# Kernel optimization log

Measured on AMD Instinct MI355X. Metric: run time of the kernel, lower is better.

## Reference

```python
import jax, jax.numpy as jnp
import numpy as np

HEADS = 8
DIM_HEAD = 64
QUERY_DIM = 1024
CONTEXT_DIM = 768
INNER = HEADS * DIM_HEAD  # 512


def setup_inputs() -> dict:
    key = jax.random.key(0)
    ks = jax.random.split(key, 8)
    b, n, j = 4, 2048, 2048
    x = jax.random.normal(ks[0], (b, n, QUERY_DIM), dtype=jnp.float32)
    context = jax.random.normal(ks[1], (b, j, CONTEXT_DIM), dtype=jnp.float32)
    mask = jax.random.randint(ks[2], (b, j), 0, 2).astype(jnp.bool_)
    # weights stored as (in, out) so forward is x @ W (torch Linear stores transpose)
    W_q = jax.random.normal(ks[3], (QUERY_DIM, INNER), dtype=jnp.float32) / np.sqrt(QUERY_DIM)
    W_k = jax.random.normal(ks[4], (CONTEXT_DIM, INNER), dtype=jnp.float32) / np.sqrt(CONTEXT_DIM)
    W_v = jax.random.normal(ks[5], (CONTEXT_DIM, INNER), dtype=jnp.float32) / np.sqrt(CONTEXT_DIM)
    W_o = jax.random.normal(ks[6], (INNER, QUERY_DIM), dtype=jnp.float32) / np.sqrt(INNER)
    b_o = jax.random.normal(ks[7], (QUERY_DIM,), dtype=jnp.float32) * 0.01
    return {"x": x, "context": context, "mask": mask,
            "W_q": W_q, "W_k": W_k, "W_v": W_v, "W_o": W_o, "b_o": b_o}


def reference(x, context, mask, W_q, W_k, W_v, W_o, b_o):
    b, n, _ = x.shape
    j = context.shape[1]
    scale = DIM_HEAD ** -0.5
    # projections -> [b, n, h, d]
    q = (x @ W_q).reshape(b, n, HEADS, DIM_HEAD)
    k = (context @ W_k).reshape(b, j, HEADS, DIM_HEAD)
    v = (context @ W_v).reshape(b, j, HEADS, DIM_HEAD)
    # similarity [b, h, n, j]
    sim = jnp.einsum('bihd,bjhd->bhij', q, k) * scale
    max_neg = -jnp.finfo(sim.dtype).max
    sim = jnp.where(mask[:, None, None, :], sim, max_neg)
    attn = jax.nn.softmax(sim, axis=-1)
    out = jnp.einsum('bhij,bjhd->bihd', attn, v).reshape(b, n, INNER)
    return out @ W_o + b_o  # dropout is identity (p=0 / eval)
```

## Files before the change

### kernel.cpp

```cpp
#include <hip/hip_runtime.h>
#include <hip/hip_bf16.h>

typedef __attribute__((ext_vector_type(4)))  float  f32x4;
typedef __attribute__((ext_vector_type(16))) float  f32x16;
typedef __attribute__((ext_vector_type(8)))  short  bf16x8;
typedef __attribute__((ext_vector_type(4)))  int    int32x4;
typedef __attribute__((ext_vector_type(2)))  unsigned int uint32x2;

#define DEVINL static __device__ __forceinline__
#define GAS __attribute__((address_space(1)))
#define LAS __attribute__((address_space(3)))

DEVINL ushort f2bf(float f) {
  unsigned u = __builtin_bit_cast(unsigned, f);
  unsigned r = u + 0x7fffu + ((u >> 16) & 1u);
  return (ushort)(r >> 16);
}

DEVINL unsigned cvtpk(float lo, float hi) {
  unsigned r;
  asm("v_cvt_pk_bf16_f32 %0, %1, %2" : "=v"(r) : "v"(lo), "v"(hi));
  return r;
}

DEVINL void plswap(unsigned &a, unsigned &b) {
  asm("v_permlane32_swap_b32 %0, %1" : "+v"(a), "+v"(b));
}

DEVINL float fexp2(float x) { return __builtin_amdgcn_exp2f(x); }

DEVINL float bf2f(short s) {
  return __builtin_bit_cast(float, ((unsigned)(ushort)s) << 16);
}

DEVINL f32x4 mfma16(bf16x8 a, bf16x8 b, f32x4 c) {
  return __builtin_amdgcn_mfma_f32_16x16x32_bf16(a, b, c, 0, 0, 0);
}
DEVINL f32x16 mfma32(bf16x8 a, bf16x8 b, f32x16 c) {
  return __builtin_amdgcn_mfma_f32_32x32x16_bf16(a, b, c, 0, 0, 0);
}

__global__ __launch_bounds__(256)
void prep_k(const float* __restrict__ x, const float* __restrict__ ctx,
            ushort* __restrict__ xb, ushort* __restrict__ cb,
            const int* __restrict__ msk, float* __restrict__ mbias,
            const float* __restrict__ Wq, const float* __restrict__ Wk,
            const float* __restrict__ Wv, const float* __restrict__ Wo,
            ushort* __restrict__ WqT, ushort* __restrict__ WkT,
            ushort* __restrict__ WvT, ushort* __restrict__ WoT)
{
  __shared__ ushort Ts[64][72];
  int id = blockIdx.x;
  if (id < 448) {
    const float* src; ushort* dst; int Kd, Nd, lid;
    if (id < 128)      { src = Wq; dst = WqT; Kd = 1024; Nd = 512;  lid = id; }
    else if (id < 224) { src = Wk; dst = WkT; Kd = 768;  Nd = 512;  lid = id - 128; }
    else if (id < 320) { src = Wv; dst = WvT; Kd = 768;  Nd = 512;  lid = id - 224; }
    else               { src = Wo; dst = WoT; Kd = 512;  Nd = 1024; lid = id - 320; }
    const int sh = (Nd == 512) ? 3 : 4;
    const int kb = lid >> sh, nb = lid & ((1 << sh) - 1);
    const int k0 = kb * 64, n0 = nb * 64;
    const int t = threadIdx.x;
    const int r = t >> 2, c0 = (t & 3) * 16;

    const float* sp = src + (size_t)(k0 + r) * Nd + n0 + c0;
    f32x4 v0 = *(const f32x4*)(sp);
    f32x4 v1 = *(const f32x4*)(sp + 4);
    f32x4 v2 = *(const f32x4*)(sp + 8);
    f32x4 v3 = *(const f32x4*)(sp + 12);
    #pragma unroll
    for (int e = 0; e < 4; e++) {
      Ts[c0 + e][r]      = f2bf(v0[e]);
      Ts[c0 + 4 + e][r]  = f2bf(v1[e]);
      Ts[c0 + 8 + e][r]  = f2bf(v2[e]);
      Ts[c0 + 12 + e][r] = f2bf(v3[e]);
    }
    __syncthreads();
    const int n = t >> 2, kc = (t & 3) * 16;
    bf16x8 o0 = *(const bf16x8*)&Ts[n][kc];
    bf16x8 o1 = *(const bf16x8*)&Ts[n][kc + 8];
    ushort* dp = dst + (size_t)(n0 + n) * Kd + k0 + kc;
    *(bf16x8*)dp       = o0;
    *(bf16x8*)(dp + 8) = o1;
    return;
  }

  const int NX = 8388608, NC = 6291456;
  int tid = (id - 448) * 256 + threadIdx.x;
  if (tid < 8192) mbias[tid] = msk[tid] ? 0.f : -1e30f;
  for (int i = tid; i < (NX + NC) / 8; i += 2048 * 256) {
    int e = i * 8;
    const float* s; ushort* d;
    if (e < NX) { s = x + e; d = xb + e; }
    else        { s = ctx + (e - NX); d = cb + (e - NX); }
    f32x4 v0 = *(const f32x4*)s;
    f32x4 v1 = *(const f32x4*)(s + 4);
    union { unsigned u[4]; int32x4 v; } pk;
    pk.u[0] = cvtpk(v0[0], v0[1]);
    pk.u[1] = cvtpk(v0[2], v0[3]);
    pk.u[2] = cvtpk(v1[0], v1[1]);
    pk.u[3] = cvtpk(v1[2], v1[3]);
    *(int32x4*)d = pk.v;
  }
}

template<int PHASE>
__global__ __launch_bounds__(256)
void mm_k(const ushort* __restrict__ xb, const ushort* __restrict__ cb,
          const ushort* __restrict__ WqT, const ushort* __restrict__ WkT,
          const ushort* __restrict__ WvT,
          ushort* __restrict__ Qb, ushort* __restrict__ Kb, ushort* __restrict__ VT,
          const ushort* __restrict__ AO, const ushort* __restrict__ WoT,
          float* __restrict__ out, const float* __restrict__ bias)
{
  __shared__ ushort As[2][128 * 32];
  __shared__ ushort Bs[2][128 * 32];

  const ushort* A; const ushort* BT; ushort* Cw = nullptr;
  int Kd, mode, m0, n0;
  if (PHASE == 0) {
    int id = blockIdx.x;
    id = (id & 7) * 96 + (id >> 3);
    const int which = id >> 8, local = id & 255;
    m0 = (local >> 2) * 128; n0 = (local & 3) * 128;
    if (which == 0)      { A = xb; BT = WqT; Cw = Qb; Kd = 1024; mode = 1; }
    else if (which == 1) { A = cb; BT = WkT; Cw = Kb; Kd = 768;  mode = 1; }
    else                 { A = cb; BT = WvT; Cw = VT; Kd = 768;  mode = 2; }
  } else {
    int id = blockIdx.x;
    id = (id & 7) * 64 + (id >> 3);
    m0 = (id >> 3) * 128; n0 = (id & 7) * 128;
    A = AO; BT = WoT; Kd = 512; mode = 0;
  }

  const int t = threadIdx.x, lane = t & 63, w = t >> 6;
  const int wr = w >> 1, wc = w & 1;
  const int g = lane >> 4, ql = lane & 15;

  const int srowo = 16 * w + (lane >> 2);
  const int sgg = (lane & 3) ^ ((lane >> 3) & 3);

  f32x4 acc[4][4];
  #pragma unroll
  for (int i = 0; i < 4; i++)
    #pragma unroll
    for (int j = 0; j < 4; j++) acc[i][j] = (f32x4){0.f, 0.f, 0.f, 0.f};

  auto stage = [&](int buf, int k0) {
    #pragma unroll
    for (int i = 0; i < 2; i++) {
      const int row = i * 64 + srowo;
      const ushort* asrc = A + (size_t)(m0 + row) * Kd + k0 + sgg * 8;
      __builtin_amdgcn_global_load_lds((const GAS void*)asrc,
          (LAS void*)&As[buf][(i * 64 + 16 * w) * 32], 16, 0, 0);
      const ushort* bsrc = BT + (size_t)(n0 + row) * Kd + k0 + sgg * 8;
      __builtin_amdgcn_global_load_lds((const GAS void*)bsrc,
          (LAS void*)&Bs[buf][(i * 64 + 16 * w) * 32], 16, 0, 0);
    }
  };

  const int NK = Kd >> 5;
  stage(0, 0);
  __syncthreads();

  const int sel = (ql >> 1) & 3;
  const int koff = (g ^ sel) * 8;

  for (int tt = 0; tt < NK; tt++) {
    const int cur = tt & 1;
    if (tt + 1 < NK) stage(cur ^ 1, (tt + 1) * 32);

    bf16x8 af[4], bfr[4];
    #pragma unroll
    for (int i = 0; i < 4; i++) {
      af[i]  = *(const bf16x8*)&As[cur][(wr * 64 + i * 16 + ql) * 32 + koff];
      bfr[i] = *(const bf16x8*)&Bs[cur][(wc * 64 + i * 16 + ql) * 32 + koff];
    }
    #pragma unroll
    for (int i = 0; i < 4; i++)
      #pragma unroll
      for (int j = 0; j < 4; j++)
        acc[i][j] = mfma16(af[i], bfr[j], acc[i][j]);
    __syncthreads();
  }

  #pragma unroll
  for (int i = 0; i < 4; i++) {
    #pragma unroll
    for (int j = 0; j < 4; j++) {
      int col = n0 + wc * 64 + j * 16 + ql;
      #pragma unroll
      for (int r = 0; r < 4; r++) {
        int mrow = m0 + wr * 64 + i * 16 + g * 4 + r;
        float v = acc[i][j][r];
        if (PHASE == 1) {
          out[(size_t)mrow * 1024 + col] = v + bias[col];
        } else {
          int b = mrow >> 11, nn = mrow & 2047;
          int hh = col >> 6, dd = col & 63;
          size_t base = (size_t)(b * 8 + hh) * 131072;
          if (mode == 1) Cw[base + (size_t)nn * 64 + dd]   = f2bf(v);
          else           Cw[base + (size_t)dd * 2048 + nn] = f2bf(v);
        }
      }
    }
  }
}

__global__ __launch_bounds__(512)
void attn_k(const ushort* __restrict__ Qb, const ushort* __restrict__ Kb,
            const ushort* __restrict__ VT, const float* __restrict__ mb,
            ushort* __restrict__ Opart, float2* __restrict__ Ml)
{
  constexpr int CHUNK = 512, NT = CHUNK / 64;
  __shared__ ushort Ks[2][64 * 64];
  __shared__ ushort Vs[2][64 * 64];

  const int bh = blockIdx.x, b = bh >> 3;
  const int sp = blockIdx.z;
  const int jb = sp * CHUNK;
  const int t = threadIdx.x, lane = t & 63, w = t >> 6;
  const int l31 = lane & 31, hi = lane >> 5;
  const int q0 = blockIdx.y * 256 + w * 32;

  const ushort* Qh = Qb + (size_t)bh * 131072;
  const ushort* Kh = Kb + (size_t)bh * 131072;
  const ushort* Vh = VT + (size_t)bh * 131072;
  const float* mp = mb + b * 2048 + 4 * hi;

  const int srow = lane >> 3;
  const int soff = ((lane & 7) * 16) ^ ((srow & 7) << 4);

  auto stage = [&](int buf, int j0) {
    const char* kg = (const char*)Kh + ((size_t)(j0 + 8 * w + srow)) * 128 + soff;
    __builtin_amdgcn_global_load_lds((const GAS void*)kg,
        (LAS void*)&Ks[buf][8 * w * 64], 16, 0, 0);
    const char* vg = (const char*)Vh + ((size_t)(8 * w + srow)) * 4096 + (size_t)j0 * 2 + soff;
    __builtin_amdgcn_global_load_lds((const GAS void*)vg,
        (LAS void*)&Vs[buf][8 * w * 64], 16, 0, 0);
  };

  bf16x8 qf[4];
  #pragma unroll
  for (int kk = 0; kk < 4; kk++)
    qf[kk] = *(const bf16x8*)(Qh + (size_t)(q0 + l31) * 64 + kk * 16 + 8 * hi);

  union { unsigned u[4]; bf16x8 v; } ones;
  ones.u[0] = 0x3F803F80u; ones.u[1] = 0x3F803F80u;
  ones.u[2] = 0x3F803F80u; ones.u[3] = 0x3F803F80u;

  f32x16 o0 = {}, o1 = {};
  float m = -1e30f, lsum = 0.f;
  const float sc = 0.18033688011112042f;

  stage(0, jb);
  __syncthreads();

  for (int tt = 0; tt < NT; ++tt) {
    const int cur = tt & 1;
    if (tt + 1 < NT) stage(cur ^ 1, jb + (tt + 1) * 64);

    #pragma unroll
    for (int js = 0; js < 2; ++js) {
      const int jloc = js * 32;
      const int j0 = jb + tt * 64 + jloc;

      f32x4 mb0 = *(const f32x4*)(mp + j0);
      f32x4 mb1 = *(const f32x4*)(mp + j0 + 8);
      f32x4 mb2 = *(const f32x4*)(mp + j0 + 16);
      f32x4 mb3 = *(const f32x4*)(mp + j0 + 24);

      const int krow = jloc + l31;
      const unsigned rsw = (unsigned)((l31 & 7) << 4);
      const char* kbase = (const char*)&Ks[cur][0] + krow * 128;
      bf16x8 kf0 = *(const bf16x8*)(kbase + ((0  + hi * 16) ^ rsw));
      bf16x8 kf1 = *(const bf16x8*)(kbase + ((32 + hi * 16) ^ rsw));
      bf16x8 kf2 = *(const bf16x8*)(kbase + ((64 + hi * 16) ^ rsw));
      bf16x8 kf3 = *(const bf16x8*)(kbase + ((96 + hi * 16) ^ rsw));

      __builtin_amdgcn_s_setprio(1);
      f32x16 z = {};
      f32x16 s = mfma32(kf0, qf[0], z);
      s = mfma32(kf1, qf[1], s);
      s = mfma32(kf2, qf[2], s);
      s = mfma32(kf3, qf[3], s);
      __builtin_amdgcn_s_setprio(0);

      const char* vb0 = (const char*)&Vs[cur][0] + l31 * 128;
      const char* vb1 = vb0 + 32 * 128;
      const unsigned vc0 = (unsigned)((jloc * 2 + hi * 16) ^ rsw);
      const unsigned vc1 = (unsigned)((jloc * 2 + 32 + hi * 16) ^ rsw);
      bf16x8 vf00 = *(const bf16x8*)(vb0 + vc0);
      bf16x8 vf01 = *(const bf16x8*)(vb0 + vc1);
      bf16x8 vf10 = *(const bf16x8*)(vb1 + vc0);
      bf16x8 vf11 = *(const bf16x8*)(vb1 + vc1);

      float pv[16];
      #pragma unroll
      for (int e = 0; e < 4; e++) {
        pv[e]      = fmaf(s[e],      sc, mb0[e]);
        pv[4 + e]  = fmaf(s[4 + e],  sc, mb1[e]);
        pv[8 + e]  = fmaf(s[8 + e],  sc, mb2[e]);
        pv[12 + e] = fmaf(s[12 + e], sc, mb3[e]);
      }

      float t0 = fmaxf(fmaxf(pv[0],  pv[1]),  pv[2]);
      float t1 = fmaxf(fmaxf(pv[3],  pv[4]),  pv[5]);
      float t2 = fmaxf(fmaxf(pv[6],  pv[7]),  pv[8]);
      float t3 = fmaxf(fmaxf(pv[9],  pv[10]), pv[11]);
      float t4 = fmaxf(fmaxf(pv[12], pv[13]), pv[14]);
      float pm = fmaxf(fmaxf(fmaxf(t0, t1), t2), fmaxf(fmaxf(t3, t4), pv[15]));
      pm = fmaxf(pm, __shfl_xor(pm, 32));

      if (!__all(pm <= m + 8.f)) {
        float mn = fmaxf(m, pm);
        float al = fexp2(m - mn);
        lsum *= al;
        #pragma unroll
        for (int r = 0; r < 16; r++) { o0[r] *= al; o1[r] *= al; }
        m = mn;
      }

      #pragma unroll
      for (int r = 0; r < 16; r++) pv[r] = fexp2(pv[r] - m);

      unsigned pk01 = cvtpk(pv[0],  pv[1]),  pk23 = cvtpk(pv[2],  pv[3]);
      unsigned pk45 = cvtpk(pv[4],  pv[5]),  pk67 = cvtpk(pv[6],  pv[7]);
      unsigned pk89 = cvtpk(pv[8],  pv[9]),  pkAB = cvtpk(pv[10], pv[11]);
      unsigned pkCD = cvtpk(pv[12], pv[13]), pkEF = cvtpk(pv[14], pv[15]);
      plswap(pk01, pk45);
      plswap(pk23, pk67);
      plswap(pk89, pkCD);
      plswap(pkAB, pkEF);
      union { unsigned u[4]; bf16x8 v; } pf0, pf1;
      pf0.u[0] = pk01; pf0.u[1] = pk23; pf0.u[2] = pk45; pf0.u[3] = pk67;
      pf1.u[0] = pk89; pf1.u[1] = pkAB; pf1.u[2] = pkCD; pf1.u[3] = pkEF;

      __builtin_amdgcn_s_setprio(1);
      f32x16 zs = {};
      zs = mfma32(ones.v, pf0.v, zs);
      zs = mfma32(ones.v, pf1.v, zs);
      o0 = mfma32(vf00, pf0.v, o0);
      o0 = mfma32(vf01, pf1.v, o0);
      o1 = mfma32(vf10, pf0.v, o1);
      o1 = mfma32(vf11, pf1.v, o1);
      __builtin_amdgcn_s_setprio(0);
      lsum += zs[0];
    }
    __syncthreads();
  }

  float inv = lsum > 0.f ? 1.0f / lsum : 0.f;
  const int q = q0 + l31;
  ushort* op = Opart + (size_t)sp * 4194304 + ((size_t)(bh * 2048 + q)) * 64;
  #pragma unroll
  for (int grp = 0; grp < 4; grp++) {
    int d0 = grp * 8 + 4 * hi;
    uint32x2 w0, w1;
    w0[0] = cvtpk(o0[4 * grp] * inv, o0[4 * grp + 1] * inv);
    w0[1] = cvtpk(o0[4 * grp + 2] * inv, o0[4 * grp + 3] * inv);
    w1[0] = cvtpk(o1[4 * grp] * inv, o1[4 * grp + 1] * inv);
    w1[1] = cvtpk(o1[4 * grp + 2] * inv, o1[4 * grp + 3] * inv);
    *(uint32x2*)(op + d0)      = w0;
    *(uint32x2*)(op + 32 + d0) = w1;
  }
  if (hi == 0) {
    float2 v; v.x = m; v.y = lsum;
    Ml[sp * 65536 + bh * 2048 + q] = v;
  }
}

__global__ __launch_bounds__(256)
void reduce_k(const ushort* __restrict__ Opart, const float2* __restrict__ Ml,
              ushort* __restrict__ AO)
{
  const int idx = blockIdx.x * 256 + threadIdx.x;
  const int d8 = idx & 7, q = (idx >> 3) & 2047, bh = idx >> 14;
  const int b = bh >> 3, h = bh & 7;

  float2 ml[4];
  float M = -1e30f;
  #pragma unroll
  for (int s = 0; s < 4; s++) {
    ml[s] = Ml[s * 65536 + bh * 2048 + q];
    M = fmaxf(M, ml[s].x);
  }
  float wgt[4], L = 0.f;
  #pragma unroll
  for (int s = 0; s < 4; s++) {
    wgt[s] = ml[s].y * fexp2(ml[s].x - M);
    L += wgt[s];
  }
  float invL = 1.f / L;

  float acc[8] = {0.f,0.f,0.f,0.f,0.f,0.f,0.f,0.f};
  #pragma unroll
  for (int s = 0; s < 4; s++) {
    bf16x8 v = *(const bf16x8*)(Opart + (size_t)s * 4194304 +
                                ((size_t)(bh * 2048 + q)) * 64 + d8 * 8);
    float ws = wgt[s] * invL;
    #pragma unroll
    for (int e = 0; e < 8; e++) acc[e] += ws * bf2f(v[e]);
  }

  union { unsigned u[4]; int32x4 v; } pk;
  pk.u[0] = cvtpk(acc[0], acc[1]);
  pk.u[1] = cvtpk(acc[2], acc[3]);
  pk.u[2] = cvtpk(acc[4], acc[5]);
  pk.u[3] = cvtpk(acc[6], acc[7]);
  *(int32x4*)(AO + ((size_t)(b * 2048 + q)) * 512 + h * 64 + d8 * 8) = pk.v;
}

extern "C" void kernel_launch(void* const* d_in, const int* in_sizes, int n_in,
                              void* d_out, int out_size, void* d_ws, size_t ws_size,
                              hipStream_t stream)
{
  const float* x   = (const float*)d_in[0];
  const float* ctx = (const float*)d_in[1];
  const int*   mk  = (const int*)d_in[2];
  const float* Wq  = (const float*)d_in[3];
  const float* Wk  = (const float*)d_in[4];
  const float* Wv  = (const float*)d_in[5];
  const float* Wo  = (const float*)d_in[6];
  const float* bo  = (const float*)d_in[7];
  float* out = (float*)d_out;

  ushort* Qb  = (ushort*)d_ws;
  ushort* Kb  = Qb + 4194304;
  ushort* VT  = Kb + 4194304;
  ushort* WoT = VT + 4194304;
  float*  mb  = (float*)(WoT + 524288);
  ushort* R2  = WoT + 524288 + 16384;
  ushort* xb  = R2;
  ushort* cb  = xb + 8388608;
  ushort* WqT = cb + 6291456;
  ushort* WkT = WqT + 524288;
  ushort* WvT = WkT + 393216;
  ushort* Opart = R2;
  float2* Ml    = (float2*)(R2 + 16777216);
  ushort* AO    = Qb;

  prep_k<<<2496, 256, 0, stream>>>(x, ctx, xb, cb, mk, mb,
                                   Wq, Wk, Wv, Wo, WqT, WkT, WvT, WoT);
  mm_k<0><<<768, 256, 0, stream>>>(xb, cb, WqT, WkT, WvT, Qb, Kb, VT,
                                   nullptr, nullptr, nullptr, nullptr);
  attn_k<<<dim3(32, 8, 4), 512, 0, stream>>>(Qb, Kb, VT, mb, Opart, Ml);
  reduce_k<<<2048, 256, 0, stream>>>(Opart, Ml, AO);
  mm_k<1><<<512, 256, 0, stream>>>(nullptr, nullptr, nullptr, nullptr, nullptr,
                                   nullptr, nullptr, nullptr, AO, WoT, out, bo);
}
```

Baseline: 148.3 us.

## Fuse fp32-to-bf16 activation conversion into projection GEMM A-tile loading

Removes the separate pass that converted x and context to bf16 in prep_k. The phase-0 GEMM now loads fp32 activations directly into registers, converts them with packed cvt instructions, and writes them to a padded LDS tile after the MFMA work, with register prefetch for the next k-step. This drops a full write and re-read of the bf16 activation buffers. In exchange, the GEMM reads twice the bytes for A, which are now read once per N-tile (4 times for Q/K/V) instead of once in the conversion pass. It also uses more registers and replaces async global-to-LDS loads for A with synchronous ones.

```diff
diff --git a/kernel.cpp b/kernel.cpp
--- a/kernel.cpp
+++ b/kernel.cpp
@@ -41,9 +41,7 @@
 }
 
 __global__ __launch_bounds__(256)
-void prep_k(const float* __restrict__ x, const float* __restrict__ ctx,
-            ushort* __restrict__ xb, ushort* __restrict__ cb,
-            const int* __restrict__ msk, float* __restrict__ mbias,
+void prep_k(const int* __restrict__ msk, float* __restrict__ mbias,
             const float* __restrict__ Wq, const float* __restrict__ Wk,
             const float* __restrict__ Wv, const float* __restrict__ Wo,
             ushort* __restrict__ WqT, ushort* __restrict__ WkT,
@@ -51,92 +49,79 @@
 {
   __shared__ ushort Ts[64][72];
   int id = blockIdx.x;
-  if (id < 448) {
-    const float* src; ushort* dst; int Kd, Nd, lid;
-    if (id < 128)      { src = Wq; dst = WqT; Kd = 1024; Nd = 512;  lid = id; }
-    else if (id < 224) { src = Wk; dst = WkT; Kd = 768;  Nd = 512;  lid = id - 128; }
-    else if (id < 320) { src = Wv; dst = WvT; Kd = 768;  Nd = 512;  lid = id - 224; }
-    else               { src = Wo; dst = WoT; Kd = 512;  Nd = 1024; lid = id - 320; }
-    const int sh = (Nd == 512) ? 3 : 4;
-    const int kb = lid >> sh, nb = lid & ((1 << sh) - 1);
-    const int k0 = kb * 64, n0 = nb * 64;
-    const int t = threadIdx.x;
-    const int r = t >> 2, c0 = (t & 3) * 16;
-
-    const float* sp = src + (size_t)(k0 + r) * Nd + n0 + c0;
-    f32x4 v0 = *(const f32x4*)(sp);
-    f32x4 v1 = *(const f32x4*)(sp + 4);
-    f32x4 v2 = *(const f32x4*)(sp + 8);
-    f32x4 v3 = *(const f32x4*)(sp + 12);
-    #pragma unroll
-    for (int e = 0; e < 4; e++) {
-      Ts[c0 + e][r]      = f2bf(v0[e]);
-      Ts[c0 + 4 + e][r]  = f2bf(v1[e]);
-      Ts[c0 + 8 + e][r]  = f2bf(v2[e]);
-      Ts[c0 + 12 + e][r] = f2bf(v3[e]);
-    }
-    __syncthreads();
-    const int n = t >> 2, kc = (t & 3) * 16;
-    bf16x8 o0 = *(const bf16x8*)&Ts[n][kc];
-    bf16x8 o1 = *(const bf16x8*)&Ts[n][kc + 8];
-    ushort* dp = dst + (size_t)(n0 + n) * Kd + k0 + kc;
-    *(bf16x8*)dp       = o0;
-    *(bf16x8*)(dp + 8) = o1;
+  if (id >= 448) {
+    int tid = (id - 448) * 256 + threadIdx.x;
+    if (tid < 8192) mbias[tid] = msk[tid] ? 0.f : -1e30f;
     return;
   }
-
-  const int NX = 8388608, NC = 6291456;
-  int tid = (id - 448) * 256 + threadIdx.x;
-  if (tid < 8192) mbias[tid] = msk[tid] ? 0.f : -1e30f;
-  for (int i = tid; i < (NX + NC) / 8; i += 2048 * 256) {
-    int e = i * 8;
-    const float* s; ushort* d;
-    if (e < NX) { s = x + e; d = xb + e; }
-    else        { s = ctx + (e - NX); d = cb + (e - NX); }
-    f32x4 v0 = *(const f32x4*)s;
-    f32x4 v1 = *(const f32x4*)(s + 4);
-    union { unsigned u[4]; int32x4 v; } pk;
-    pk.u[0] = cvtpk(v0[0], v0[1]);
-    pk.u[1] = cvtpk(v0[2], v0[3]);
-    pk.u[2] = cvtpk(v1[0], v1[1]);
-    pk.u[3] = cvtpk(v1[2], v1[3]);
-    *(int32x4*)d = pk.v;
-  }
+  const float* src; ushort* dst; int Kd, Nd, lid;
+  if (id < 128)      { src = Wq; dst = WqT; Kd = 1024; Nd = 512;  lid = id; }
+  else if (id < 224) { src = Wk; dst = WkT; Kd = 768;  Nd = 512;  lid = id - 128; }
+  else if (id < 320) { src = Wv; dst = WvT; Kd = 768;  Nd = 512;  lid = id - 224; }
+  else               { src = Wo; dst = WoT; Kd = 512;  Nd = 1024; lid = id - 320; }
+  const int sh = (Nd == 512) ? 3 : 4;
+  const int kb = lid >> sh, nb = lid & ((1 << sh) - 1);
+  const int k0 = kb * 64, n0 = nb * 64;
+  const int t = threadIdx.x;
+  const int r = t >> 2, c0 = (t & 3) * 16;
+
+  const float* sp = src + (size_t)(k0 + r) * Nd + n0 + c0;
+  f32x4 v0 = *(const f32x4*)(sp);
+  f32x4 v1 = *(const f32x4*)(sp + 4);
+  f32x4 v2 = *(const f32x4*)(sp + 8);
+  f32x4 v3 = *(const f32x4*)(sp + 12);
+  #pragma unroll
+  for (int e = 0; e < 4; e++) {
+    Ts[c0 + e][r]      = f2bf(v0[e]);
+    Ts[c0 + 4 + e][r]  = f2bf(v1[e]);
+    Ts[c0 + 8 + e][r]  = f2bf(v2[e]);
+    Ts[c0 + 12 + e][r] = f2bf(v3[e]);
+  }
+  __syncthreads();
+  const int n = t >> 2, kc = (t & 3) * 16;
+  bf16x8 o0 = *(const bf16x8*)&Ts[n][kc];
+  bf16x8 o1 = *(const bf16x8*)&Ts[n][kc + 8];
+  ushort* dp = dst + (size_t)(n0 + n) * Kd + k0 + kc;
+  *(bf16x8*)dp       = o0;
+  *(bf16x8*)(dp + 8) = o1;
 }
 
 template<int PHASE>
 __global__ __launch_bounds__(256)
-void mm_k(const ushort* __restrict__ xb, const ushort* __restrict__ cb,
+void mm_k(const float* __restrict__ xf, const float* __restrict__ cf,
           const ushort* __restrict__ WqT, const ushort* __restrict__ WkT,
           const ushort* __restrict__ WvT,
           ushort* __restrict__ Qb, ushort* __restrict__ Kb, ushort* __restrict__ VT,
           const ushort* __restrict__ AO, const ushort* __restrict__ WoT,
           float* __restrict__ out, const float* __restrict__ bias)
 {
-  __shared__ ushort As[2][128 * 32];
+  constexpr int AST = (PHASE == 0) ? 40 : 32;
+  __shared__ ushort As[2][128 * AST];
   __shared__ ushort Bs[2][128 * 32];
 
-  const ushort* A; const ushort* BT; ushort* Cw = nullptr;
+  const float* Af = nullptr; const ushort* Ab = nullptr; const ushort* BT;
+  ushort* Cw = nullptr;
   int Kd, mode, m0, n0;
   if (PHASE == 0) {
     int id = blockIdx.x;
     id = (id & 7) * 96 + (id >> 3);
     const int which = id >> 8, local = id & 255;
     m0 = (local >> 2) * 128; n0 = (local & 3) * 128;
-    if (which == 0)      { A = xb; BT = WqT; Cw = Qb; Kd = 1024; mode = 1; }
-    else if (which == 1) { A = cb; BT = WkT; Cw = Kb; Kd = 768;  mode = 1; }
-    else                 { A = cb; BT = WvT; Cw = VT; Kd = 768;  mode = 2; }
+    if (which == 0)      { Af = xf; BT = WqT; Cw = Qb; Kd = 1024; mode = 1; }
+    else if (which == 1) { Af = cf; BT = WkT; Cw = Kb; Kd = 768;  mode = 1; }
+    else                 { Af = cf; BT = WvT; Cw = VT; Kd = 768;  mode = 2; }
   } else {
     int id = blockIdx.x;
     id = (id & 7) * 64 + (id >> 3);
     m0 = (id >> 3) * 128; n0 = (id & 7) * 128;
-    A = AO; BT = WoT; Kd = 512; mode = 0;
+    Ab = AO; BT = WoT; Kd = 512; mode = 0;
   }
 
   const int t = threadIdx.x, lane = t & 63, w = t >> 6;
   const int wr = w >> 1, wc = w & 1;
   const int g = lane >> 4, ql = lane & 15;
 
+  const int arow = t >> 1, akc = (t & 1) * 16;
   const int srowo = 16 * w + (lane >> 2);
   const int sgg = (lane & 3) ^ ((lane >> 3) & 3);
 
@@ -146,21 +131,49 @@
     #pragma unroll
     for (int j = 0; j < 4; j++) acc[i][j] = (f32x4){0.f, 0.f, 0.f, 0.f};
 
-  auto stage = [&](int buf, int k0) {
+  auto stageB = [&](int buf, int k0) {
     #pragma unroll
     for (int i = 0; i < 2; i++) {
       const int row = i * 64 + srowo;
-      const ushort* asrc = A + (size_t)(m0 + row) * Kd + k0 + sgg * 8;
-      __builtin_amdgcn_global_load_lds((const GAS void*)asrc,
-          (LAS void*)&As[buf][(i * 64 + 16 * w) * 32], 16, 0, 0);
       const ushort* bsrc = BT + (size_t)(n0 + row) * Kd + k0 + sgg * 8;
       __builtin_amdgcn_global_load_lds((const GAS void*)bsrc,
           (LAS void*)&Bs[buf][(i * 64 + 16 * w) * 32], 16, 0, 0);
     }
   };
+  auto stageA_lds = [&](int buf, int k0) {
+    #pragma unroll
+    for (int i = 0; i < 2; i++) {
+      const int row = i * 64 + srowo;
+      const ushort* asrc = Ab + (size_t)(m0 + row) * Kd + k0 + sgg * 8;
+      __builtin_amdgcn_global_load_lds((const GAS void*)asrc,
+          (LAS void*)&As[buf][(i * 64 + 16 * w) * 32], 16, 0, 0);
+    }
+  };
+  auto writeA_f32 = [&](int buf, const f32x4& v0, const f32x4& v1,
+                        const f32x4& v2, const f32x4& v3) {
+    union { unsigned u[4]; int32x4 v; } w1_, w2_;
+    w1_.u[0] = cvtpk(v0[0], v0[1]); w1_.u[1] = cvtpk(v0[2], v0[3]);
+    w1_.u[2] = cvtpk(v1[0], v1[1]); w1_.u[3] = cvtpk(v1[2], v1[3]);
+    w2_.u[0] = cvtpk(v2[0], v2[1]); w2_.u[1] = cvtpk(v2[2], v2[3]);
+    w2_.u[2] = cvtpk(v3[0], v3[1]); w2_.u[3] = cvtpk(v3[2], v3[3]);
+    ushort* dst = &As[buf][arow * 40 + akc];
+    *(int32x4*)dst       = w1_.v;
+    *(int32x4*)(dst + 8) = w2_.v;
+  };
 
   const int NK = Kd >> 5;
-  stage(0, 0);
+  if (PHASE == 0) {
+    const float* ap = Af + (size_t)(m0 + arow) * Kd + akc;
+    f32x4 v0 = *(const f32x4*)(ap);
+    f32x4 v1 = *(const f32x4*)(ap + 4);
+    f32x4 v2 = *(const f32x4*)(ap + 8);
+    f32x4 v3 = *(const f32x4*)(ap + 12);
+    writeA_f32(0, v0, v1, v2, v3);
+    stageB(0, 0);
+  } else {
+    stageA_lds(0, 0);
+    stageB(0, 0);
+  }
   __syncthreads();
 
   const int sel = (ql >> 1) & 3;
@@ -168,12 +181,29 @@
 
   for (int tt = 0; tt < NK; tt++) {
     const int cur = tt & 1;
-    if (tt + 1 < NK) stage(cur ^ 1, (tt + 1) * 32);
+    const bool pre = (tt + 1 < NK);
+
+    f32x4 n0v, n1v, n2v, n3v;
+    if (PHASE == 0) {
+      if (pre) {
+        const float* ap = Af + (size_t)(m0 + arow) * Kd + (tt + 1) * 32 + akc;
+        n0v = *(const f32x4*)(ap);
+        n1v = *(const f32x4*)(ap + 4);
+        n2v = *(const f32x4*)(ap + 8);
+        n3v = *(const f32x4*)(ap + 12);
+        stageB(cur ^ 1, (tt + 1) * 32);
+      }
+    } else {
+      if (pre) { stageA_lds(cur ^ 1, (tt + 1) * 32); stageB(cur ^ 1, (tt + 1) * 32); }
+    }
 
     bf16x8 af[4], bfr[4];
     #pragma unroll
     for (int i = 0; i < 4; i++) {
-      af[i]  = *(const bf16x8*)&As[cur][(wr * 64 + i * 16 + ql) * 32 + koff];
+      if (PHASE == 0)
+        af[i] = *(const bf16x8*)&As[cur][(wr * 64 + i * 16 + ql) * 40 + g * 8];
+      else
+        af[i] = *(const bf16x8*)&As[cur][(wr * 64 + i * 16 + ql) * 32 + koff];
       bfr[i] = *(const bf16x8*)&Bs[cur][(wc * 64 + i * 16 + ql) * 32 + koff];
     }
     #pragma unroll
@@ -181,6 +211,8 @@
       #pragma unroll
       for (int j = 0; j < 4; j++)
         acc[i][j] = mfma16(af[i], bfr[j], acc[i][j]);
+
+    if (PHASE == 0 && pre) writeA_f32(cur ^ 1, n0v, n1v, n2v, n3v);
     __syncthreads();
   }
 
@@ -431,18 +463,15 @@
   ushort* WoT = VT + 4194304;
   float*  mb  = (float*)(WoT + 524288);
   ushort* R2  = WoT + 524288 + 16384;
-  ushort* xb  = R2;
-  ushort* cb  = xb + 8388608;
-  ushort* WqT = cb + 6291456;
+  ushort* WqT = R2;
   ushort* WkT = WqT + 524288;
   ushort* WvT = WkT + 393216;
-  ushort* Opart = R2;
-  float2* Ml    = (float2*)(R2 + 16777216);
+  ushort* Opart = WvT + 393216;
+  float2* Ml    = (float2*)(Opart + 16777216);
   ushort* AO    = Qb;
 
-  prep_k<<<2496, 256, 0, stream>>>(x, ctx, xb, cb, mk, mb,
-                                   Wq, Wk, Wv, Wo, WqT, WkT, WvT, WoT);
-  mm_k<0><<<768, 256, 0, stream>>>(xb, cb, WqT, WkT, WvT, Qb, Kb, VT,
+  prep_k<<<480, 256, 0, stream>>>(mk, mb, Wq, Wk, Wv, Wo, WqT, WkT, WvT, WoT);
+  mm_k<0><<<768, 256, 0, stream>>>(x, ctx, WqT, WkT, WvT, Qb, Kb, VT,
                                    nullptr, nullptr, nullptr, nullptr);
   attn_k<<<dim3(32, 8, 4), 512, 0, stream>>>(Qb, Kb, VT, mb, Opart, Ml);
   reduce_k<<<2048, 256, 0, stream>>>(Opart, Ml, AO);
```

After: 143.0 us. 3.6% less time.
